# Kernel optimization log

Measured on AMD Instinct MI355X. Metric: run time of the kernel, lower is better.

## Reference

```python
import jax, jax.numpy as jnp
import numpy as np

EMBED = 256
HID = EMBED * 4
NUM_EXPERTS = 4
WINDOW = 16
B, T = 4, 4096
EPS = 1e-5


def _ln(x, g, b):
    m = jnp.mean(x, axis=-1, keepdims=True)
    v = jnp.mean(jnp.square(x - m), axis=-1, keepdims=True)
    return (x - m) / jnp.sqrt(v + EPS) * g + b


def setup_inputs() -> dict:
    key = jax.random.key(0)
    ks = jax.random.split(key, 16)
    s = 0.02
    d = {
        'x': jax.random.normal(ks[0], (B, T, EMBED), jnp.float32),
        'ln1_g': jnp.ones((EMBED,), jnp.float32),
        'ln1_b': jnp.zeros((EMBED,), jnp.float32),
        'qkv_w': jax.random.normal(ks[1], (EMBED, 3 * EMBED), jnp.float32) * s,
        'qkv_b': jnp.zeros((3 * EMBED,), jnp.float32),
        'proj_w': jax.random.normal(ks[2], (EMBED, EMBED), jnp.float32) * s,
        'proj_b': jnp.zeros((EMBED,), jnp.float32),
        'attn_gate': jnp.ones((EMBED,), jnp.float32),
        'ln2_g': jnp.ones((EMBED,), jnp.float32),
        'ln2_b': jnp.zeros((EMBED,), jnp.float32),
        'gating_w': jax.random.normal(ks[3], (EMBED, NUM_EXPERTS), jnp.float32) * s,
        'gating_b': jnp.zeros((NUM_EXPERTS,), jnp.float32),
        'e_w1': jax.random.normal(ks[4], (NUM_EXPERTS, EMBED, HID), jnp.float32) * s,
        'e_b1': jnp.zeros((NUM_EXPERTS, HID), jnp.float32),
        'e_w2': jax.random.normal(ks[5], (NUM_EXPERTS, HID, EMBED), jnp.float32) * s,
        'e_b2': jnp.zeros((NUM_EXPERTS, EMBED), jnp.float32),
    }
    return d


def reference(x, ln1_g, ln1_b, qkv_w, qkv_b, proj_w, proj_b, attn_gate,
              ln2_g, ln2_b, gating_w, gating_b, e_w1, e_b1, e_w2, e_b2):
    Bx, Tx, C = x.shape
    # --- sparse attention branch ---
    h = _ln(x, ln1_g, ln1_b)
    qkv = h @ qkv_w + qkv_b                      # [B,T,3C]
    q, k, v = jnp.split(qkv, 3, axis=-1)
    scores = jnp.einsum('btc,bsc->bts', q, k) / jnp.sqrt(jnp.float32(C))
    idx = jnp.arange(Tx)
    diff = idx[:, None] - idx[None, :]           # i - j
    in_window = (diff >= 0) & (diff <= WINDOW)
    # faithful to torch code: scores outside the window (but causal) stay 0,
    # positions above the diagonal become -inf; softmax over full row
    scores = jnp.where(in_window, scores, 0.0)
    scores = jnp.where(diff >= 0, scores, -jnp.inf)
    att = jax.nn.softmax(scores, axis=-1)        # [B,T,T]
    a_out = jnp.einsum('bts,bsc->btc', att, v) * attn_gate
    x = x + a_out @ proj_w + proj_b
    # --- dense all-expert MoE branch ---
    h2 = _ln(x, ln2_g, ln2_b)
    gates = jax.nn.softmax(h2 @ gating_w + gating_b, axis=-1)     # [B,T,E]
    hid = jax.nn.gelu(jnp.einsum('btc,ech->bteh', h2, e_w1) + e_b1,
                      approximate=False)                           # [B,T,E,H]
    eo = jnp.einsum('bteh,eho->bteo', hid, e_w2) + e_b2            # [B,T,E,C]
    moe_out = jnp.einsum('bte,bteo->bto', gates, eo)
    return x + moe_out
```

## Files before the change

kernel.cpp:

```cpp
#include <hip/hip_runtime.h>
#include <hip/hip_bf16.h>
#include <math.h>

#define T_   4096
#define B_   4
#define C_   256
#define C3_  768
#define H_   1024
#define E_   4
#define M_   (B_*T_)
#define NCH_ 64
#define CHL_ (T_/NCH_)
#define KH_  4096

typedef __attribute__((ext_vector_type(8))) short short8;
typedef __attribute__((ext_vector_type(4))) float floatx4;

__device__ __forceinline__ float b2f(unsigned short u) {
  union { unsigned int i; float f; } x; x.i = ((unsigned int)u) << 16; return x.f;
}
__device__ __forceinline__ unsigned short f2b(float f) {
  __hip_bfloat16 h = __float2bfloat16(f);
  return *reinterpret_cast<unsigned short*>(&h);
}
__device__ __forceinline__ void unpack8(uint4 a, float* f) {
  unsigned int w[4] = {a.x, a.y, a.z, a.w};
  #pragma unroll
  for (int i = 0; i < 4; i++) {
    union { unsigned int u; float g; } lo, hi;
    lo.u = w[i] << 16; hi.u = w[i] & 0xffff0000u;
    f[2*i] = lo.g; f[2*i+1] = hi.g;
  }
}
__device__ __forceinline__ void gl_lds16(const void* g, void* l) {
  __builtin_amdgcn_global_load_lds(
      (const __attribute__((address_space(1))) void*)g,
      (__attribute__((address_space(3))) void*)l, 16, 0, 0);
}
__device__ __forceinline__ float gelu_s(float v) {
  float e = __expf(-1.702f * v);
  return v * __builtin_amdgcn_rcpf(1.0f + e);
}
__device__ __forceinline__ unsigned int pk_fp8x4(float a, float b, float c, float d) {
  unsigned int v = 0;
  v = __builtin_amdgcn_cvt_pk_fp8_f32(a, b, v, false);
  v = __builtin_amdgcn_cvt_pk_fp8_f32(c, d, v, true);
  return v;
}
__device__ __forceinline__ unsigned char f2fp8(float v) {
  return (unsigned char)(__builtin_amdgcn_cvt_pk_fp8_f32(v, v, 0, false) & 0xff);
}
__device__ __forceinline__ float sel4(float4 v, int e) {
  float r = v.x;
  r = (e == 1) ? v.y : r;
  r = (e == 2) ? v.z : r;
  r = (e == 3) ? v.w : r;
  return r;
}

__global__ __launch_bounds__(256) void transpose_cvt(
    const float* __restrict__ src, unsigned short* __restrict__ dst, int K, int N,
    int dstLd, size_t dstZStride) {
  __shared__ float tile[32][33];
  src += (size_t)blockIdx.z * K * N;
  dst += (size_t)blockIdx.z * dstZStride;
  int n0 = blockIdx.x * 32, k0 = blockIdx.y * 32;
  int tx = threadIdx.x, ty = threadIdx.y;
  #pragma unroll
  for (int i = 0; i < 32; i += 8)
    tile[ty + i][tx] = src[(size_t)(k0 + ty + i) * N + n0 + tx];
  __syncthreads();
  #pragma unroll
  for (int i = 0; i < 32; i += 8)
    dst[(size_t)(n0 + ty + i) * dstLd + k0 + tx] = f2b(tile[tx][ty + i]);
}

__global__ __launch_bounds__(256) void transpose_w2_fp8(
    const float* __restrict__ src, unsigned char* __restrict__ dst) {
  __shared__ float tile[32][33];
  int e = blockIdx.z;
  src += (size_t)e * H_ * C_;
  int h0 = blockIdx.x * 32, c0 = blockIdx.y * 32;
  int tx = threadIdx.x, ty = threadIdx.y;
  #pragma unroll
  for (int i = 0; i < 32; i += 8)
    tile[ty + i][tx] = src[(size_t)(h0 + ty + i) * C_ + c0 + tx];
  __syncthreads();
  int k = e * H_ + h0 + tx;
  int chunk = k >> 6, kc = k & 63;
  #pragma unroll
  for (int i = 0; i < 32; i += 8) {
    int c = c0 + ty + i;
    int sw = ((((kc >> 4) ^ ((c >> 2) & 3)) << 4) | (kc & 15));
    dst[((size_t)chunk * 256 + c) * 64 + sw] = f2fp8(tile[tx][ty + i] * 256.0f);
  }
}

__global__ __launch_bounds__(256) void ln1_kernel(
    const float* __restrict__ x, const float* __restrict__ g,
    const float* __restrict__ b, unsigned short* __restrict__ h) {
  __shared__ float red[4];
  int row = blockIdx.x, tid = threadIdx.x;
  float v = x[(size_t)row * C_ + tid];
  float s = v;
  #pragma unroll
  for (int o = 32; o; o >>= 1) s += __shfl_xor(s, o);
  if ((tid & 63) == 0) red[tid >> 6] = s;
  __syncthreads();
  float mean = (red[0] + red[1] + red[2] + red[3]) * (1.0f / C_);
  __syncthreads();
  float d = v - mean;
  float q = d * d;
  #pragma unroll
  for (int o = 32; o; o >>= 1) q += __shfl_xor(q, o);
  if ((tid & 63) == 0) red[tid >> 6] = q;
  __syncthreads();
  float var = (red[0] + red[1] + red[2] + red[3]) * (1.0f / C_);
  h[(size_t)row * C_ + tid] = f2b(d * rsqrtf(var + 1e-5f) * g[tid] + b[tid]);
}

__global__ __launch_bounds__(256) void ln2_gates_kernel(
    const float* __restrict__ x1, const float* __restrict__ g,
    const float* __restrict__ b, const float* __restrict__ gw,
    const float* __restrict__ gb, unsigned short* __restrict__ h2,
    float* __restrict__ gates) {
  __shared__ float red[4];
  __shared__ float redg[4][4];
  int row = blockIdx.x, tid = threadIdx.x;
  float v = x1[(size_t)row * C_ + tid];
  float s = v;
  #pragma unroll
  for (int o = 32; o; o >>= 1) s += __shfl_xor(s, o);
  if ((tid & 63) == 0) red[tid >> 6] = s;
  __syncthreads();
  float mean = (red[0] + red[1] + red[2] + red[3]) * (1.0f / C_);
  __syncthreads();
  float d = v - mean;
  float q = d * d;
  #pragma unroll
  for (int o = 32; o; o >>= 1) q += __shfl_xor(q, o);
  if ((tid & 63) == 0) red[tid >> 6] = q;
  __syncthreads();
  float var = (red[0] + red[1] + red[2] + red[3]) * (1.0f / C_);
  float hv = d * rsqrtf(var + 1e-5f) * g[tid] + b[tid];
  h2[(size_t)row * C_ + tid] = f2b(hv);
  float p0 = hv * gw[tid * 4 + 0];
  float p1 = hv * gw[tid * 4 + 1];
  float p2 = hv * gw[tid * 4 + 2];
  float p3 = hv * gw[tid * 4 + 3];
  #pragma unroll
  for (int o = 32; o; o >>= 1) {
    p0 += __shfl_xor(p0, o); p1 += __shfl_xor(p1, o);
    p2 += __shfl_xor(p2, o); p3 += __shfl_xor(p3, o);
  }
  if ((tid & 63) == 0) {
    int w = tid >> 6;
    redg[w][0] = p0; redg[w][1] = p1; redg[w][2] = p2; redg[w][3] = p3;
  }
  __syncthreads();
  if (tid == 0) {
    float t4[4];
    #pragma unroll
    for (int e = 0; e < 4; e++)
      t4[e] = redg[0][e] + redg[1][e] + redg[2][e] + redg[3][e] + gb[e];
    float m = fmaxf(fmaxf(t4[0], t4[1]), fmaxf(t4[2], t4[3]));
    float zs = 0.f;
    #pragma unroll
    for (int e = 0; e < 4; e++) { t4[e] = __expf(t4[e] - m); zs += t4[e]; }
    float inv = 1.0f / zs;
    #pragma unroll
    for (int e = 0; e < 4; e++) gates[(size_t)row * 4 + e] = t4[e] * inv;
  }
}

__global__ __launch_bounds__(256) void scan1_kernel(const unsigned short* __restrict__ qkv,
                                                    float* __restrict__ S) {
  int b = blockIdx.x >> 6, ch = blockIdx.x & 63, c = threadIdx.x;
  float s = 0.f;
  size_t base = ((size_t)b * T_ + (size_t)ch * CHL_) * C3_ + 512 + c;
  for (int t = 0; t < CHL_; t++) s += b2f(qkv[base + (size_t)t * C3_]);
  S[((size_t)b * NCH_ + ch) * C_ + c] = s;
}
__global__ __launch_bounds__(256) void scan2_kernel(float* __restrict__ S) {
  int b = blockIdx.x, c = threadIdx.x;
  float run = 0.f;
  for (int ch = 0; ch < NCH_; ch++) {
    size_t i = ((size_t)b * NCH_ + ch) * C_ + c;
    float t = S[i]; S[i] = run; run += t;
  }
}
__global__ __launch_bounds__(256) void scan3_kernel(const unsigned short* __restrict__ qkv,
                                                    const float* __restrict__ S,
                                                    unsigned short* __restrict__ Pb) {
  int b = blockIdx.x >> 6, ch = blockIdx.x & 63, c = threadIdx.x;
  float run = S[((size_t)b * NCH_ + ch) * C_ + c];
  size_t row0 = (size_t)b * T_ + (size_t)ch * CHL_;
  for (int t = 0; t < CHL_; t++) {
    run += b2f(qkv[(row0 + t) * C3_ + 512 + c]);
    Pb[(row0 + t) * C_ + c] = f2b(run);
  }
}

__global__ __launch_bounds__(256) void attn_kernel(
    const unsigned short* __restrict__ qkv, const unsigned short* __restrict__ Pb,
    const float* __restrict__ gate, unsigned short* __restrict__ aout) {
  int wave = threadIdx.x >> 6, lane = threadIdx.x & 63;
  int r = blockIdx.x * 4 + wave;
  int t = r & (T_ - 1);
  int g = lane >> 4, u = lane & 15;
  const unsigned short* qp = qkv + (size_t)r * C3_ + (u << 4);
  float qv[16];
  unpack8(*(const uint4*)qp, qv);
  unpack8(*(const uint4*)(qp + 8), qv + 8);
  float sc[5];
  #pragma unroll
  for (int rnd = 0; rnd < 5; rnd++) {
    int j = rnd * 4 + g;
    int jj = t - 16 + j;
    bool valid = (j <= 16) && (jj >= 0);
    float d = 0.f;
    if (valid) {
      const unsigned short* kp = qkv + (size_t)(r - 16 + j) * C3_ + 256 + (u << 4);
      float kv[16];
      unpack8(*(const uint4*)kp, kv);
      unpack8(*(const uint4*)(kp + 8), kv + 8);
      #pragma unroll
      for (int c = 0; c < 16; c++) d += qv[c] * kv[c];
    }
    d += __shfl_xor(d, 1); d += __shfl_xor(d, 2);
    d += __shfl_xor(d, 4); d += __shfl_xor(d, 8);
    sc[rnd] = valid ? d * 0.0625f : -1e30f;
  }
  float m = fmaxf(fmaxf(fmaxf(sc[0], sc[1]), fmaxf(sc[2], sc[3])), sc[4]);
  m = fmaxf(m, __shfl_xor(m, 16));
  m = fmaxf(m, __shfl_xor(m, 32));
  if (t > 16) m = fmaxf(m, 0.0f);
  float ev[5], Zp = 0.f;
  #pragma unroll
  for (int rnd = 0; rnd < 5; rnd++) {
    ev[rnd] = (sc[rnd] > -1e29f) ? __expf(sc[rnd] - m) : 0.f;
    Zp += ev[rnd];
  }
  Zp += __shfl_xor(Zp, 16);
  Zp += __shfl_xor(Zp, 32);
  float e0v = 0.f;
  if (t > 16) { e0v = __expf(-m); Zp += e0v * (float)(t - 16); }
  float vp[16];
  #pragma unroll
  for (int c = 0; c < 16; c++) vp[c] = 0.f;
  #pragma unroll
  for (int rnd = 0; rnd < 5; rnd++) {
    if (ev[rnd] != 0.f) {
      int j = rnd * 4 + g;
      const unsigned short* vpp = qkv + (size_t)(r - 16 + j) * C3_ + 512 + (u << 4);
      float vv[16];
      unpack8(*(const uint4*)vpp, vv);
      unpack8(*(const uint4*)(vpp + 8), vv + 8);
      #pragma unroll
      for (int c = 0; c < 16; c++) vp[c] += ev[rnd] * vv[c];
    }
  }
  #pragma unroll
  for (int c = 0; c < 16; c++) {
    vp[c] += __shfl_xor(vp[c], 16);
    vp[c] += __shfl_xor(vp[c], 32);
  }
  if (g == 0) {
    if (t > 16) {
      const unsigned short* pp = Pb + (size_t)(r - 17) * C_ + (u << 4);
      float pv[16];
      unpack8(*(const uint4*)pp, pv);
      unpack8(*(const uint4*)(pp + 8), pv + 8);
      #pragma unroll
      for (int c = 0; c < 16; c++) vp[c] += e0v * pv[c];
    }
    float inv = 1.0f / Zp;
    const float* gp = gate + (u << 4);
    unsigned int ow[8];
    #pragma unroll
    for (int i = 0; i < 8; i++) {
      unsigned short lo = f2b(vp[2*i] * inv * gp[2*i]);
      unsigned short hi = f2b(vp[2*i+1] * inv * gp[2*i+1]);
      ow[i] = (unsigned int)lo | ((unsigned int)hi << 16);
    }
    uint4 s0 = {ow[0], ow[1], ow[2], ow[3]};
    uint4 s1 = {ow[4], ow[5], ow[6], ow[7]};
    *(uint4*)(aout + (size_t)r * C_ + (u << 4)) = s0;
    *(uint4*)(aout + (size_t)r * C_ + (u << 4) + 8) = s1;
  }
}

template<int EPI>
__global__ __launch_bounds__(256) void gemm128(
    const unsigned short* __restrict__ A, const unsigned short* __restrict__ Bt,
    const float* __restrict__ bias, int K, int ldOut,
    const float* __restrict__ resid, float* __restrict__ outf,
    unsigned short* __restrict__ outb) {
  __shared__ __align__(16) unsigned short As[128 * 64];
  __shared__ __align__(16) unsigned short Bs[128 * 64];
  const int tid = threadIdx.x;
  const int wave = tid >> 6, lane = tid & 63;
  const int mBlk = blockIdx.x * 128, nBlk = blockIdx.y * 128;
  const int wm = (wave >> 1) * 64, wn = (wave & 1) * 64;
  const int lm = lane & 15, lk = (lane >> 4) * 8;
  floatx4 acc[4][4];
  #pragma unroll
  for (int i = 0; i < 4; i++)
    #pragma unroll
    for (int j = 0; j < 4; j++) acc[i][j] = (floatx4){0.f, 0.f, 0.f, 0.f};

  for (int kt = 0; kt < K; kt += 64) {
    __syncthreads();
    #pragma unroll
    for (int i = 0; i < 4; i++) {
      int seg = i * 256 + tid;
      int row = seg >> 3, g = seg & 7;
      int gc = (g ^ (row & 7)) << 3;
      gl_lds16(A + (size_t)(mBlk + row) * K + kt + gc, &As[seg * 8]);
      gl_lds16(Bt + (size_t)(nBlk + row) * K + kt + gc, &Bs[seg * 8]);
    }
    __syncthreads();
    #pragma unroll
    for (int kk = 0; kk < 64; kk += 32) {
      short8 mf[4], nf[4];
      #pragma unroll
      for (int j = 0; j < 4; j++) {
        int row = wm + j * 16 + lm;
        mf[j] = *(const short8*)&As[row * 64 + ((((kk + lk) >> 3) ^ (row & 7)) << 3)];
      }
      #pragma unroll
      for (int i = 0; i < 4; i++) {
        int row = wn + i * 16 + lm;
        nf[i] = *(const short8*)&Bs[row * 64 + ((((kk + lk) >> 3) ^ (row & 7)) << 3)];
      }
      #pragma unroll
      for (int i = 0; i < 4; i++)
        #pragma unroll
        for (int j = 0; j < 4; j++)
          acc[i][j] = __builtin_amdgcn_mfma_f32_16x16x32_bf16(nf[i], mf[j], acc[i][j], 0, 0, 0);
    }
  }
  const int lc = lane & 15, quad = lane >> 4, q4 = quad * 4;
  #pragma unroll
  for (int i = 0; i < 4; i++) {
    int n0 = nBlk + wn + i * 16 + q4;
    float4 bs = *(const float4*)&bias[n0];
    #pragma unroll
    for (int j = 0; j < 4; j++) {
      int m = mBlk + wm + j * 16 + lc;
      float v0 = acc[i][j][0] + bs.x, v1 = acc[i][j][1] + bs.y;
      float v2 = acc[i][j][2] + bs.z, v3 = acc[i][j][3] + bs.w;
      if (EPI == 0) {
        ushort4 o = {f2b(v0), f2b(v1), f2b(v2), f2b(v3)};
        *(ushort4*)&outb[(size_t)m * ldOut + n0] = o;
      } else {
        size_t idx = (size_t)m * ldOut + n0;
        float4 r = *(const float4*)&resid[idx];
        float4 o = {v0 + r.x, v1 + r.y, v2 + r.z, v3 + r.w};
        *(float4*)&outf[idx] = o;
      }
    }
  }
}

__global__ __launch_bounds__(512, 2) void moe_fused(
    const unsigned short* __restrict__ h2,
    const unsigned short* __restrict__ w1t,
    const float* __restrict__ b1,
    const unsigned char* __restrict__ w2b,
    const float* __restrict__ b2,
    const float* __restrict__ gates,
    const float* __restrict__ x1,
    float* __restrict__ out) {
  __shared__ __align__(16) unsigned short W1s[2][64 * 256];
  __shared__ __align__(16) unsigned char  W2s[2][256 * 64];
  __shared__ __align__(16) unsigned char  Hs[2][64 * 64];
  __shared__ __align__(16) float          B1s[2][64];
  const int tid = threadIdx.x;
  const int wave = tid >> 6, lane = tid & 63;
  const int lm = lane & 15, quad = lane >> 4;
  const int mb = blockIdx.x * 64;
  const bool isUp = wave < 4;
  const int uw = wave & 3;
  const int wmu = (uw >> 1) * 32;
  const int whu = (uw & 1) * 32;
  const int wc  = uw * 64;

  auto stageW1 = [&](int c, int buf) {
    const unsigned short* ws = w1t + (size_t)c * 64 * C_;
    #pragma unroll
    for (int t = 0; t < 4; t++) {
      int seg = t * 512 + tid;
      int row = seg >> 5, g = seg & 31;
      int gp = (g & 24) | ((g & 7) ^ (row & 7));
      gl_lds16(ws + (size_t)row * C_ + gp * 8, &W1s[buf][seg * 8]);
    }
    if (lane < 16)
      gl_lds16(b1 + (size_t)c * 64 + lane * 4, &B1s[buf][0]);
  };
  auto stageW2 = [&](int c, int buf) {
    const unsigned char* vs = w2b + (size_t)c * 256 * 64;
    #pragma unroll
    for (int t = 0; t < 2; t++) {
      int seg = t * 512 + tid;
      gl_lds16(vs + (size_t)seg * 16, &W2s[buf][seg * 16]);
    }
  };

  stageW1(0, 0);

  short8 af[8][2];
  float4 ga[2];
  if (isUp) {
    #pragma unroll
    for (int kk = 0; kk < 8; kk++) {
      int kc = kk * 4 + quad;
      #pragma unroll
      for (int j = 0; j < 2; j++) {
        int row = mb + wmu + j * 16 + lm;
        af[kk][j] = *(const short8*)(h2 + (size_t)row * C_ + kc * 8);
      }
    }
    #pragma unroll
    for (int j = 0; j < 2; j++)
      ga[j] = *(const float4*)(gates + (size_t)(mb + wmu + j * 16 + lm) * 4);
  }

  floatx4 dacc[4][4];
  #pragma unroll
  for (int i = 0; i < 4; i++)
    #pragma unroll
    for (int j = 0; j < 4; j++) dacc[i][j] = (floatx4){0.f, 0.f, 0.f, 0.f};

  asm volatile("s_waitcnt vmcnt(0)" ::: "memory");

  for (int c = 0; c < 64; c++) {
    const int wb = c & 1;
    __builtin_amdgcn_s_barrier();
    __builtin_amdgcn_sched_barrier(0);
    stageW1((c + 1) & 63, wb ^ 1);
    stageW2(c, wb);

    if (isUp) {
      floatx4 uacc[2][2];
      #pragma unroll
      for (int i = 0; i < 2; i++)
        #pragma unroll
        for (int j = 0; j < 2; j++) uacc[i][j] = (floatx4){0.f, 0.f, 0.f, 0.f};
      __builtin_amdgcn_s_setprio(1);
      #pragma unroll
      for (int kk = 0; kk < 8; kk++) {
        int kc = kk * 4 + quad;
        short8 nf[2];
        #pragma unroll
        for (int i = 0; i < 2; i++) {
          int row = whu + i * 16 + lm;
          nf[i] = *(const short8*)&W1s[wb][row * 256 + ((kc ^ (row & 7)) << 3)];
        }
        #pragma unroll
        for (int i = 0; i < 2; i++)
          #pragma unroll
          for (int j = 0; j < 2; j++)
            uacc[i][j] = __builtin_amdgcn_mfma_f32_16x16x32_bf16(nf[i], af[kk][j], uacc[i][j], 0, 0, 0);
      }
      __builtin_amdgcn_s_setprio(0);
      int e = c >> 4;
      float gs0 = 64.0f * sel4(ga[0], e);
      float gs1 = 64.0f * sel4(ga[1], e);
      #pragma unroll
      for (int i = 0; i < 2; i++) {
        float4 bb = *(const float4*)&B1s[wb][whu + i * 16 + quad * 4];
        #pragma unroll
        for (int j = 0; j < 2; j++) {
          float gs = j ? gs1 : gs0;
          unsigned int w = pk_fp8x4(gs * gelu_s(uacc[i][j][0] + bb.x),
                                    gs * gelu_s(uacc[i][j][1] + bb.y),
                                    gs * gelu_s(uacc[i][j][2] + bb.z),
                                    gs * gelu_s(uacc[i][j][3] + bb.w));
          int m = wmu + j * 16 + lm;
          int hh = whu + i * 16 + quad * 4;
          *(unsigned int*)&Hs[wb][m * 64 + ((((hh >> 3) ^ (m & 7)) << 3) | (hh & 7))] = w;
        }
      }
      asm volatile("s_waitcnt lgkmcnt(0)" ::: "memory");
    } else if (c > 0) {
      const int pb = wb ^ 1;
      __builtin_amdgcn_s_setprio(1);
      #pragma unroll
      for (int kk = 0; kk < 2; kk++) {
        long mfh[4], nfw[4];
        #pragma unroll
        for (int j = 0; j < 4; j++) {
          int m = j * 16 + lm;
          int g8 = quad + 4 * kk;
          mfh[j] = *(const long*)&Hs[pb][m * 64 + ((g8 ^ (m & 7)) << 3)];
        }
        #pragma unroll
        for (int i = 0; i < 4; i++) {
          int cr = wc + i * 16 + lm;
          int sl = ((quad >> 1) + 2 * kk) ^ ((cr >> 2) & 3);
          nfw[i] = *(const long*)&W2s[pb][cr * 64 + (sl << 4) + ((quad & 1) << 3)];
        }
        #pragma unroll
        for (int i = 0; i < 4; i++)
          #pragma unroll
          for (int j = 0; j < 4; j++)
            dacc[i][j] = __builtin_amdgcn_mfma_f32_16x16x32_fp8_fp8(nfw[i], mfh[j], dacc[i][j], 0, 0, 0);
      }
      __builtin_amdgcn_s_setprio(0);
    }
    asm volatile("s_waitcnt vmcnt(0)" ::: "memory");
  }

  __builtin_amdgcn_s_barrier();
  __builtin_amdgcn_sched_barrier(0);
  if (!isUp) {
    #pragma unroll
    for (int kk = 0; kk < 2; kk++) {
      long mfh[4], nfw[4];
      #pragma unroll
      for (int j = 0; j < 4; j++) {
        int m = j * 16 + lm;
        int g8 = quad + 4 * kk;
        mfh[j] = *(const long*)&Hs[1][m * 64 + ((g8 ^ (m & 7)) << 3)];
      }
      #pragma unroll
      for (int i = 0; i < 4; i++) {
        int cr = wc + i * 16 + lm;
        int sl = ((quad >> 1) + 2 * kk) ^ ((cr >> 2) & 3);
        nfw[i] = *(const long*)&W2s[1][cr * 64 + (sl << 4) + ((quad & 1) << 3)];
      }
      #pragma unroll
      for (int i = 0; i < 4; i++)
        #pragma unroll
        for (int j = 0; j < 4; j++)
          dacc[i][j] = __builtin_amdgcn_mfma_f32_16x16x32_fp8_fp8(nfw[i], mfh[j], dacc[i][j], 0, 0, 0);
    }
    const float sc = 1.0f / 16384.0f;
    const int q4 = quad * 4;
    #pragma unroll
    for (int j = 0; j < 4; j++) {
      int m = mb + j * 16 + lm;
      float4 g4 = *(const float4*)(gates + (size_t)m * 4);
      #pragma unroll
      for (int i = 0; i < 4; i++) {
        int n0 = wc + i * 16 + q4;
        float4 bA = *(const float4*)&b2[0 * C_ + n0];
        float4 bB = *(const float4*)&b2[1 * C_ + n0];
        float4 bC = *(const float4*)&b2[2 * C_ + n0];
        float4 bD = *(const float4*)&b2[3 * C_ + n0];
        size_t idx = (size_t)m * C_ + n0;
        float4 r = *(const float4*)&x1[idx];
        float4 o;
        o.x = dacc[i][j][0]*sc + r.x + g4.x*bA.x + g4.y*bB.x + g4.z*bC.x + g4.w*bD.x;
        o.y = dacc[i][j][1]*sc + r.y + g4.x*bA.y + g4.y*bB.y + g4.z*bC.y + g4.w*bD.y;
        o.z = dacc[i][j][2]*sc + r.z + g4.x*bA.z + g4.y*bB.z + g4.z*bC.z + g4.w*bD.z;
        o.w = dacc[i][j][3]*sc + r.w + g4.x*bA.w + g4.y*bB.w + g4.z*bC.w + g4.w*bD.w;
        *(float4*)&out[idx] = o;
      }
    }
  }
}

extern "C" void kernel_launch(void* const* d_in, const int* in_sizes, int n_in,
                              void* d_out, int out_size, void* d_ws, size_t ws_size,
                              hipStream_t stream) {
  const float* x       = (const float*)d_in[0];
  const float* ln1_g   = (const float*)d_in[1];
  const float* ln1_b   = (const float*)d_in[2];
  const float* qkv_w   = (const float*)d_in[3];
  const float* qkv_b   = (const float*)d_in[4];
  const float* proj_w  = (const float*)d_in[5];
  const float* proj_b  = (const float*)d_in[6];
  const float* attn_g  = (const float*)d_in[7];
  const float* ln2_g   = (const float*)d_in[8];
  const float* ln2_b   = (const float*)d_in[9];
  const float* gat_w   = (const float*)d_in[10];
  const float* gat_b   = (const float*)d_in[11];
  const float* e_w1    = (const float*)d_in[12];
  const float* e_b1    = (const float*)d_in[13];
  const float* e_w2    = (const float*)d_in[14];
  const float* e_b2    = (const float*)d_in[15];
  float* out = (float*)d_out;

  char* p = (char*)d_ws;
  unsigned short* h    = (unsigned short*)p; p += (size_t)M_ * C_ * 2;
  unsigned short* qkv  = (unsigned short*)p; p += (size_t)M_ * C3_ * 2;
  unsigned short* Pb   = (unsigned short*)p; p += (size_t)M_ * C_ * 2;
  unsigned short* aout = (unsigned short*)p; p += (size_t)M_ * C_ * 2;
  float*          x1   = (float*)p;          p += (size_t)M_ * C_ * 4;
  unsigned short* h2   = (unsigned short*)p; p += (size_t)M_ * C_ * 2;
  float*          gts  = (float*)p;          p += (size_t)M_ * E_ * 4;
  float*          S    = (float*)p;          p += (size_t)B_ * NCH_ * C_ * 4;
  unsigned short* wq   = (unsigned short*)p; p += (size_t)C3_ * C_ * 2;
  unsigned short* wp   = (unsigned short*)p; p += (size_t)C_ * C_ * 2;
  unsigned short* w1t  = (unsigned short*)p; p += (size_t)KH_ * C_ * 2;
  unsigned char*  w2f8 = (unsigned char*)p;  p += (size_t)C_ * KH_;

  dim3 t32x8(32, 8);
  transpose_cvt<<<dim3(C3_/32, C_/32, 1), t32x8, 0, stream>>>(qkv_w, wq, C_, C3_, C_, 0);
  transpose_cvt<<<dim3(C_/32, C_/32, 1),  t32x8, 0, stream>>>(proj_w, wp, C_, C_, C_, 0);
  transpose_cvt<<<dim3(H_/32, C_/32, E_), t32x8, 0, stream>>>(e_w1, w1t, C_, H_, C_, (size_t)H_ * C_);
  transpose_w2_fp8<<<dim3(H_/32, C_/32, E_), t32x8, 0, stream>>>(e_w2, w2f8);

  ln1_kernel<<<M_, 256, 0, stream>>>(x, ln1_g, ln1_b, h);
  gemm128<0><<<dim3(M_/128, C3_/128), 256, 0, stream>>>(h, wq, qkv_b, C_, C3_,
      nullptr, nullptr, qkv);
  scan1_kernel<<<B_*NCH_, 256, 0, stream>>>(qkv, S);
  scan2_kernel<<<B_, 256, 0, stream>>>(S);
  scan3_kernel<<<B_*NCH_, 256, 0, stream>>>(qkv, S, Pb);
  attn_kernel<<<M_/4, 256, 0, stream>>>(qkv, Pb, attn_g, aout);
  gemm128<1><<<dim3(M_/128, C_/128), 256, 0, stream>>>(aout, wp, proj_b, C_, C_,
      x, x1, nullptr);
  ln2_gates_kernel<<<M_, 256, 0, stream>>>(x1, ln2_g, ln2_b, gat_w, gat_b, h2, gts);
  moe_fused<<<M_/64, 512, 0, stream>>>(h2, w1t, e_b1, w2f8, e_b2, gts, x1, out);
}
```

Before: 317.3 us.

## Split MoE hidden dimension across two blocks and load W2 fragments into registers

The fused MoE kernel now splits the 4096-wide expert hidden dimension into two halves handled by separate blocks, doubling the grid to 512 blocks. Each block writes partial fp32 down-projection results, and a new reduce kernel sums them with the residual, gates and bias. W2 is pre-laid out in MFMA fragment order, so down waves load it straight into registers instead of staging through LDS. The b1 bias is read from global memory, LDS use drops and the occupancy hint rises to 4. The aim is more parallelism and less LDS traffic per block, paid for by an extra kernel launch and a round trip of the fp32 partial sums through memory.

```diff
diff --git a/kernel.cpp b/kernel.cpp
--- a/kernel.cpp
+++ b/kernel.cpp
@@ -15,6 +15,7 @@
 
 typedef __attribute__((ext_vector_type(8))) short short8;
 typedef __attribute__((ext_vector_type(4))) float floatx4;
+typedef __attribute__((ext_vector_type(2))) long long2v;
 
 __device__ __forceinline__ float b2f(unsigned short u) {
   union { unsigned int i; float f; } x; x.i = ((unsigned int)u) << 16; return x.f;
@@ -75,25 +76,20 @@
     dst[(size_t)(n0 + ty + i) * dstLd + k0 + tx] = f2b(tile[tx][ty + i]);
 }
 
-__global__ __launch_bounds__(256) void transpose_w2_fp8(
+__global__ __launch_bounds__(256) void prep_w2r(
     const float* __restrict__ src, unsigned char* __restrict__ dst) {
-  __shared__ float tile[32][33];
-  int e = blockIdx.z;
-  src += (size_t)e * H_ * C_;
-  int h0 = blockIdx.x * 32, c0 = blockIdx.y * 32;
-  int tx = threadIdx.x, ty = threadIdx.y;
-  #pragma unroll
-  for (int i = 0; i < 32; i += 8)
-    tile[ty + i][tx] = src[(size_t)(h0 + ty + i) * C_ + c0 + tx];
-  __syncthreads();
-  int k = e * H_ + h0 + tx;
-  int chunk = k >> 6, kc = k & 63;
-  #pragma unroll
-  for (int i = 0; i < 32; i += 8) {
-    int c = c0 + ty + i;
-    int sw = ((((kc >> 4) ^ ((c >> 2) & 3)) << 4) | (kc & 15));
-    dst[((size_t)chunk * 256 + c) * 64 + sw] = f2fp8(tile[tx][ty + i] * 256.0f);
-  }
+  int flat = blockIdx.x * 256 + threadIdx.x;
+  int b    = flat & 7;
+  int kh   = (flat >> 3) & 1;
+  int lane = (flat >> 4) & 63;
+  int i    = (flat >> 10) & 3;
+  int cg   = (flat >> 12) & 3;
+  int chunk= (flat >> 14) & 63;
+  int quad = lane >> 4, lm = lane & 15;
+  int e    = chunk >> 4;
+  int hL   = (chunk & 15) * 64 + kh * 32 + quad * 8 + b;
+  int c    = cg * 64 + i * 16 + lm;
+  dst[flat] = f2fp8(src[((size_t)e * H_ + hL) * C_ + c] * 256.0f);
 }
 
 __global__ __launch_bounds__(256) void ln1_kernel(
@@ -363,51 +359,39 @@
   }
 }
 
-__global__ __launch_bounds__(512, 2) void moe_fused(
+__global__ __launch_bounds__(512, 4) void moe_fused(
     const unsigned short* __restrict__ h2,
     const unsigned short* __restrict__ w1t,
     const float* __restrict__ b1,
-    const unsigned char* __restrict__ w2b,
-    const float* __restrict__ b2,
+    const unsigned char* __restrict__ w2r,
     const float* __restrict__ gates,
-    const float* __restrict__ x1,
-    float* __restrict__ out) {
+    float* __restrict__ dpart) {
   __shared__ __align__(16) unsigned short W1s[2][64 * 256];
-  __shared__ __align__(16) unsigned char  W2s[2][256 * 64];
   __shared__ __align__(16) unsigned char  Hs[2][64 * 64];
-  __shared__ __align__(16) float          B1s[2][64];
   const int tid = threadIdx.x;
   const int wave = tid >> 6, lane = tid & 63;
   const int lm = lane & 15, quad = lane >> 4;
-  const int mb = blockIdx.x * 64;
+  const int half = blockIdx.x >> 8;
+  const int mb = (blockIdx.x & 255) * 64;
+  const int g0 = half * 32;
   const bool isUp = wave < 4;
   const int uw = wave & 3;
   const int wmu = (uw >> 1) * 32;
   const int whu = (uw & 1) * 32;
   const int wc  = uw * 64;
 
-  auto stageW1 = [&](int c, int buf) {
-    const unsigned short* ws = w1t + (size_t)c * 64 * C_;
+  auto stageW1 = [&](int g, int buf) {
+    const unsigned short* ws = w1t + (size_t)g * 64 * C_;
     #pragma unroll
     for (int t = 0; t < 4; t++) {
       int seg = t * 512 + tid;
-      int row = seg >> 5, g = seg & 31;
-      int gp = (g & 24) | ((g & 7) ^ (row & 7));
+      int row = seg >> 5, gg = seg & 31;
+      int gp = (gg & 24) | ((gg & 7) ^ (row & 7));
       gl_lds16(ws + (size_t)row * C_ + gp * 8, &W1s[buf][seg * 8]);
     }
-    if (lane < 16)
-      gl_lds16(b1 + (size_t)c * 64 + lane * 4, &B1s[buf][0]);
   };
-  auto stageW2 = [&](int c, int buf) {
-    const unsigned char* vs = w2b + (size_t)c * 256 * 64;
-    #pragma unroll
-    for (int t = 0; t < 2; t++) {
-      int seg = t * 512 + tid;
-      gl_lds16(vs + (size_t)seg * 16, &W2s[buf][seg * 16]);
-    }
-  };
-
-  stageW1(0, 0);
+
+  stageW1(g0, 0);
 
   short8 af[8][2];
   float4 ga[2];
@@ -426,6 +410,7 @@
       ga[j] = *(const float4*)(gates + (size_t)(mb + wmu + j * 16 + lm) * 4);
   }
 
+  long2v w2reg[4];
   floatx4 dacc[4][4];
   #pragma unroll
   for (int i = 0; i < 4; i++)
@@ -434,12 +419,12 @@
 
   asm volatile("s_waitcnt vmcnt(0)" ::: "memory");
 
-  for (int c = 0; c < 64; c++) {
+  for (int c = 0; c < 32; c++) {
     const int wb = c & 1;
+    const int g = g0 + c;
     __builtin_amdgcn_s_barrier();
     __builtin_amdgcn_sched_barrier(0);
-    stageW1((c + 1) & 63, wb ^ 1);
-    stageW2(c, wb);
+    stageW1((g + 1) & 63, wb ^ 1);
 
     if (isUp) {
       floatx4 uacc[2][2];
@@ -464,12 +449,12 @@
             uacc[i][j] = __builtin_amdgcn_mfma_f32_16x16x32_bf16(nf[i], af[kk][j], uacc[i][j], 0, 0, 0);
       }
       __builtin_amdgcn_s_setprio(0);
-      int e = c >> 4;
+      int e = g >> 4;
       float gs0 = 64.0f * sel4(ga[0], e);
       float gs1 = 64.0f * sel4(ga[1], e);
       #pragma unroll
       for (int i = 0; i < 2; i++) {
-        float4 bb = *(const float4*)&B1s[wb][whu + i * 16 + quad * 4];
+        float4 bb = *(const float4*)&b1[(size_t)g * 64 + whu + i * 16 + quad * 4];
         #pragma unroll
         for (int j = 0; j < 2; j++) {
           float gs = j ? gs1 : gs0;
@@ -483,31 +468,31 @@
         }
       }
       asm volatile("s_waitcnt lgkmcnt(0)" ::: "memory");
-    } else if (c > 0) {
-      const int pb = wb ^ 1;
-      __builtin_amdgcn_s_setprio(1);
-      #pragma unroll
-      for (int kk = 0; kk < 2; kk++) {
-        long mfh[4], nfw[4];
+    } else {
+      if (c > 0) {
+        const int pb = wb ^ 1;
+        __builtin_amdgcn_s_setprio(1);
         #pragma unroll
-        for (int j = 0; j < 4; j++) {
-          int m = j * 16 + lm;
-          int g8 = quad + 4 * kk;
-          mfh[j] = *(const long*)&Hs[pb][m * 64 + ((g8 ^ (m & 7)) << 3)];
+        for (int kk = 0; kk < 2; kk++) {
+          long mfh[4];
+          #pragma unroll
+          for (int j = 0; j < 4; j++) {
+            int m = j * 16 + lm;
+            int g8 = quad + 4 * kk;
+            mfh[j] = *(const long*)&Hs[pb][m * 64 + ((g8 ^ (m & 7)) << 3)];
+          }
+          #pragma unroll
+          for (int i = 0; i < 4; i++)
+            #pragma unroll
+            for (int j = 0; j < 4; j++)
+              dacc[i][j] = __builtin_amdgcn_mfma_f32_16x16x32_fp8_fp8(w2reg[i][kk], mfh[j], dacc[i][j], 0, 0, 0);
         }
-        #pragma unroll
-        for (int i = 0; i < 4; i++) {
-          int cr = wc + i * 16 + lm;
-          int sl = ((quad >> 1) + 2 * kk) ^ ((cr >> 2) & 3);
-          nfw[i] = *(const long*)&W2s[pb][cr * 64 + (sl << 4) + ((quad & 1) << 3)];
-        }
-        #pragma unroll
-        for (int i = 0; i < 4; i++)
-          #pragma unroll
-          for (int j = 0; j < 4; j++)
-            dacc[i][j] = __builtin_amdgcn_mfma_f32_16x16x32_fp8_fp8(nfw[i], mfh[j], dacc[i][j], 0, 0, 0);
-      }
-      __builtin_amdgcn_s_setprio(0);
+        __builtin_amdgcn_s_setprio(0);
+      }
+      const unsigned char* vs = w2r + ((size_t)(g * 4 + uw) * 4) * 1024 + lane * 16;
+      #pragma unroll
+      for (int i = 0; i < 4; i++)
+        w2reg[i] = *(const long2v*)(vs + (size_t)i * 1024);
     }
     asm volatile("s_waitcnt vmcnt(0)" ::: "memory");
   }
@@ -517,7 +502,7 @@
   if (!isUp) {
     #pragma unroll
     for (int kk = 0; kk < 2; kk++) {
-      long mfh[4], nfw[4];
+      long mfh[4];
       #pragma unroll
       for (int j = 0; j < 4; j++) {
         int m = j * 16 + lm;
@@ -525,41 +510,46 @@
         mfh[j] = *(const long*)&Hs[1][m * 64 + ((g8 ^ (m & 7)) << 3)];
       }
       #pragma unroll
-      for (int i = 0; i < 4; i++) {
-        int cr = wc + i * 16 + lm;
-        int sl = ((quad >> 1) + 2 * kk) ^ ((cr >> 2) & 3);
-        nfw[i] = *(const long*)&W2s[1][cr * 64 + (sl << 4) + ((quad & 1) << 3)];
-      }
-      #pragma unroll
       for (int i = 0; i < 4; i++)
         #pragma unroll
         for (int j = 0; j < 4; j++)
-          dacc[i][j] = __builtin_amdgcn_mfma_f32_16x16x32_fp8_fp8(nfw[i], mfh[j], dacc[i][j], 0, 0, 0);
-    }
-    const float sc = 1.0f / 16384.0f;
+          dacc[i][j] = __builtin_amdgcn_mfma_f32_16x16x32_fp8_fp8(w2reg[i][kk], mfh[j], dacc[i][j], 0, 0, 0);
+    }
     const int q4 = quad * 4;
     #pragma unroll
     for (int j = 0; j < 4; j++) {
-      int m = mb + j * 16 + lm;
-      float4 g4 = *(const float4*)(gates + (size_t)m * 4);
+      int m = j * 16 + lm;
       #pragma unroll
       for (int i = 0; i < 4; i++) {
         int n0 = wc + i * 16 + q4;
-        float4 bA = *(const float4*)&b2[0 * C_ + n0];
-        float4 bB = *(const float4*)&b2[1 * C_ + n0];
-        float4 bC = *(const float4*)&b2[2 * C_ + n0];
-        float4 bD = *(const float4*)&b2[3 * C_ + n0];
-        size_t idx = (size_t)m * C_ + n0;
-        float4 r = *(const float4*)&x1[idx];
-        float4 o;
-        o.x = dacc[i][j][0]*sc + r.x + g4.x*bA.x + g4.y*bB.x + g4.z*bC.x + g4.w*bD.x;
-        o.y = dacc[i][j][1]*sc + r.y + g4.x*bA.y + g4.y*bB.y + g4.z*bC.y + g4.w*bD.y;
-        o.z = dacc[i][j][2]*sc + r.z + g4.x*bA.z + g4.y*bB.z + g4.z*bC.z + g4.w*bD.z;
-        o.w = dacc[i][j][3]*sc + r.w + g4.x*bA.w + g4.y*bB.w + g4.z*bC.w + g4.w*bD.w;
-        *(float4*)&out[idx] = o;
-      }
-    }
-  }
+        *(floatx4*)&dpart[((size_t)blockIdx.x * 64 + m) * C_ + n0] = dacc[i][j];
+      }
+    }
+  }
+}
+
+__global__ __launch_bounds__(256) void moe_reduce(
+    const float* __restrict__ dpart, const float* __restrict__ x1,
+    const float* __restrict__ gates, const float* __restrict__ b2,
+    float* __restrict__ out) {
+  int flat = blockIdx.x * 256 + threadIdx.x;
+  int m = flat >> 6, c0 = (flat & 63) << 2;
+  int pb = m >> 6, ml = m & 63;
+  const float sc = 1.0f / 16384.0f;
+  float4 a = *(const float4*)&dpart[((size_t)pb * 64 + ml) * C_ + c0];
+  float4 b = *(const float4*)&dpart[(((size_t)pb + 256) * 64 + ml) * C_ + c0];
+  float4 r = *(const float4*)&x1[(size_t)m * C_ + c0];
+  float4 g4 = *(const float4*)&gates[(size_t)m * 4];
+  float4 bA = *(const float4*)&b2[0 * C_ + c0];
+  float4 bB = *(const float4*)&b2[1 * C_ + c0];
+  float4 bC = *(const float4*)&b2[2 * C_ + c0];
+  float4 bD = *(const float4*)&b2[3 * C_ + c0];
+  float4 o;
+  o.x = (a.x + b.x) * sc + r.x + g4.x*bA.x + g4.y*bB.x + g4.z*bC.x + g4.w*bD.x;
+  o.y = (a.y + b.y) * sc + r.y + g4.x*bA.y + g4.y*bB.y + g4.z*bC.y + g4.w*bD.y;
+  o.z = (a.z + b.z) * sc + r.z + g4.x*bA.z + g4.y*bB.z + g4.z*bC.z + g4.w*bD.z;
+  o.w = (a.w + b.w) * sc + r.w + g4.x*bA.w + g4.y*bB.w + g4.z*bC.w + g4.w*bD.w;
+  *(float4*)&out[(size_t)m * C_ + c0] = o;
 }
 
 extern "C" void kernel_launch(void* const* d_in, const int* in_sizes, int n_in,
@@ -595,13 +585,14 @@
   unsigned short* wq   = (unsigned short*)p; p += (size_t)C3_ * C_ * 2;
   unsigned short* wp   = (unsigned short*)p; p += (size_t)C_ * C_ * 2;
   unsigned short* w1t  = (unsigned short*)p; p += (size_t)KH_ * C_ * 2;
-  unsigned char*  w2f8 = (unsigned char*)p;  p += (size_t)C_ * KH_;
+  unsigned char*  w2r  = (unsigned char*)p;  p += (size_t)C_ * KH_;
+  float*          dpart= (float*)p;          p += (size_t)512 * 64 * C_ * 4;
 
   dim3 t32x8(32, 8);
   transpose_cvt<<<dim3(C3_/32, C_/32, 1), t32x8, 0, stream>>>(qkv_w, wq, C_, C3_, C_, 0);
   transpose_cvt<<<dim3(C_/32, C_/32, 1),  t32x8, 0, stream>>>(proj_w, wp, C_, C_, C_, 0);
   transpose_cvt<<<dim3(H_/32, C_/32, E_), t32x8, 0, stream>>>(e_w1, w1t, C_, H_, C_, (size_t)H_ * C_);
-  transpose_w2_fp8<<<dim3(H_/32, C_/32, E_), t32x8, 0, stream>>>(e_w2, w2f8);
+  prep_w2r<<<4096, 256, 0, stream>>>(e_w2, w2r);
 
   ln1_kernel<<<M_, 256, 0, stream>>>(x, ln1_g, ln1_b, h);
   gemm128<0><<<dim3(M_/128, C3_/128), 256, 0, stream>>>(h, wq, qkv_b, C_, C3_,
@@ -613,5 +604,6 @@
   gemm128<1><<<dim3(M_/128, C_/128), 256, 0, stream>>>(aout, wp, proj_b, C_, C_,
       x, x1, nullptr);
   ln2_gates_kernel<<<M_, 256, 0, stream>>>(x1, ln2_g, ln2_b, gat_w, gat_b, h2, gts);
-  moe_fused<<<M_/64, 512, 0, stream>>>(h2, w1t, e_b1, w2f8, e_b2, gts, x1, out);
-}
+  moe_fused<<<512, 512, 0, stream>>>(h2, w1t, e_b1, w2r, gts, dpart);
+  moe_reduce<<<M_*64/256, 256, 0, stream>>>(dpart, x1, gts, e_b2, out);
+}
```

Result: slower. 543.4 us (+71.2%).
